# Kernel optimization log

Measured on AMD Instinct MI355X. Metric: run time of the kernel, lower is better.

Reference implementation:

```python
import jax, jax.numpy as jnp
import numpy as np
from math import sqrt

B, LT, LM = 4, 512, 1024
HID, NH, HD = 512, 8, 64          # self-attn: hidden, n_head, head_size
NHP, KS = 16, 64                  # cross-attn: 2*max_charge*n_head_per_mass, key_size
FF = 4 * HID
ALPHA = 2.0
EPS = 1e-5


def apply_rope(x, dis):
    # dis: same trailing dim as x; chunk into (sin, cos) halves
    s, c = jnp.split(dis, 2, axis=-1)
    x0, x1 = x[..., 0::2], x[..., 1::2]
    return jnp.concatenate([x0 * c - x1 * s, x1 * c + x0 * s], axis=-1)


def layer_norm(x, g, b):
    mu = jnp.mean(x, axis=-1, keepdims=True)
    var = jnp.mean(jnp.square(x - mu), axis=-1, keepdims=True)
    return (x - mu) * jax.lax.rsqrt(var + EPS) * g + b


def deep_norm(x, postx, g, b):
    # dropout is identity in eval mode
    return layer_norm(x * ALPHA + postx, g, b)


def attn_block(x_q, x_kv, dis_q, dis_k, wq, bq, wk, bk, wv, bv, wo, bo, mask, n_head, head_size):
    bsz = x_q.shape[0]
    q = (x_q @ wq.T + bq).reshape(bsz, -1, n_head, head_size)
    k = (x_kv @ wk.T + bk).reshape(bsz, -1, n_head, head_size)
    v = (x_kv @ wv.T + bv).reshape(bsz, -1, n_head, head_size)
    q = apply_rope(q, dis_q)
    k = apply_rope(k, dis_k)
    attn = jnp.einsum('bnhd,bmhd->bhnm', q, k) / sqrt(head_size)  # [B,H,Lq,Lk]
    attn = jnp.where(mask, attn, -jnp.inf)
    attn = jax.nn.softmax(attn, axis=-1)
    out = jnp.einsum('bhnm,bmhd->bnhd', attn, v).reshape(bsz, -1, n_head * head_size)
    return out @ wo.T + bo


def setup_inputs() -> dict:
    key = jax.random.key(0)
    ks = jax.random.split(key, 32)
    rn = lambda i, shape, s=1.0: jax.random.normal(ks[i], shape, jnp.float32) * s
    inp = {}
    inp['tgt'] = rn(0, (B, LT, HID))
    inp['mem'] = rn(1, (B, LM, HID))
    inp['glycan_mass'] = rn(2, (B, LT, NH, HD))
    inp['glycan_query_mass'] = rn(3, (B, LT, NH, HD))
    inp['glycan_crossattn_mass'] = rn(4, (B, LT, NHP, KS))
    inp['node_mass_emb'] = rn(5, (B, LM, NHP, KS))
    inp['node_mass'] = rn(6, (B, LM))
    causal = jnp.tril(jnp.ones((LT, LT), bool))
    inp['tgt_mask'] = jnp.broadcast_to(causal[None, None], (B, 1, LT, LT))
    inp['rel_mask'] = jnp.ones((B, 1, LT, LM), bool)
    inp['layer'] = 0
    inp['A'] = rn(7, (1,))
    w = 0.03  # param init scale
    # self-attn params
    inp['wq1'] = rn(8, (HID, HID), w);  inp['bq1'] = jnp.zeros((HID,))
    inp['wk1'] = rn(9, (HID, HID), w);  inp['bk1'] = jnp.zeros((HID,))
    inp['wv1'] = rn(10, (HID, HID), w); inp['bv1'] = jnp.zeros((HID,))
    inp['wo1'] = rn(11, (HID, HID), w); inp['bo1'] = jnp.zeros((HID,))
    inp['ln1_g'] = jnp.ones((HID,));    inp['ln1_b'] = jnp.zeros((HID,))
    # cross-attn params (projection dim NHP*KS = 1024)
    P = NHP * KS
    inp['wq2'] = rn(12, (P, HID), w);   inp['bq2'] = jnp.zeros((P,))
    inp['wk2'] = rn(13, (P, HID), w);   inp['bk2'] = jnp.zeros((P,))
    inp['wv2'] = rn(14, (P, HID), w);   inp['bv2'] = jnp.zeros((P,))
    inp['wo2'] = rn(15, (HID, P), w);   inp['bo2'] = jnp.zeros((HID,))
    inp['ln2_g'] = jnp.ones((HID,));    inp['ln2_b'] = jnp.zeros((HID,))
    # FFN params (no bias) + DeepNorm LN
    inp['w_ff1'] = rn(16, (FF, HID), w)
    inp['w_ff2'] = rn(17, (HID, FF), w)
    inp['ln3_g'] = jnp.ones((HID,));    inp['ln3_b'] = jnp.zeros((HID,))
    return inp


def reference(tgt, mem, glycan_mass, glycan_query_mass, glycan_crossattn_mass,
              node_mass_emb, node_mass, tgt_mask, rel_mask, layer, A,
              wq1, bq1, wk1, bk1, wv1, bv1, wo1, bo1, ln1_g, ln1_b,
              wq2, bq2, wk2, bk2, wv2, bv2, wo2, bo2, ln2_g, ln2_b,
              w_ff1, w_ff2, ln3_g, ln3_b):
    # masked self-attention with mass RoPE + DeepNorm
    postx = attn_block(tgt, tgt, glycan_query_mass, glycan_mass,
                       wq1, bq1, wk1, bk1, wv1, bv1, wo1, bo1,
                       tgt_mask, NH, HD)
    tgt = deep_norm(tgt, postx, ln1_g, ln1_b)
    # cross-attention with mass RoPE + DeepNorm (node_mass, layer, A unused in math)
    postx = attn_block(tgt, mem, glycan_crossattn_mass, node_mass_emb,
                       wq2, bq2, wk2, bk2, wv2, bv2, wo2, bo2,
                       rel_mask, NHP, KS)
    tgt = deep_norm(tgt, postx, ln2_g, ln2_b)
    # FFN + DeepNorm
    postx = jax.nn.relu(tgt @ w_ff1.T) @ w_ff2.T
    tgt = deep_norm(tgt, postx, ln3_g, ln3_b)
    return (tgt, A)
```

## Files before the change

kernel.cpp:

```cpp
#include <hip/hip_runtime.h>
#include <hip/hip_bf16.h>
#include <math.h>

#define EPS 1e-5f

typedef __attribute__((ext_vector_type(8))) __bf16 bf16x8;
typedef __attribute__((ext_vector_type(4))) float f32x4;

struct CvtJobs {
    const float* src[12];
    __bf16* dst[12];
    int off[13];
};

__global__ __launch_bounds__(256) void cvt_k(CvtJobs J, int total) {
    int g = blockIdx.x * 256 + threadIdx.x;
    if (g >= total) return;
    int j = 0;
    #pragma unroll
    for (int t = 0; t < 11; ++t) j += (g >= J.off[t + 1]) ? 1 : 0;
    int lg = g - J.off[j];
    const float* s = J.src[j] + (size_t)lg * 8;
    float4 a = *(const float4*)s;
    float4 b = *(const float4*)(s + 4);
    bf16x8 o;
    o[0] = (__bf16)a.x; o[1] = (__bf16)a.y; o[2] = (__bf16)a.z; o[3] = (__bf16)a.w;
    o[4] = (__bf16)b.x; o[5] = (__bf16)b.y; o[6] = (__bf16)b.z; o[7] = (__bf16)b.w;
    *(bf16x8*)(J.dst[j] + (size_t)lg * 8) = o;
}

template<int BT, int KS, typename OutT, bool RELU, bool HAS_BIAS, bool ROPE>
__global__ __launch_bounds__(256) void gemm_bf16_k(const __bf16* __restrict__ A,
                                                   const __bf16* __restrict__ W,
                                                   const float* __restrict__ b0,
                                                   const float* __restrict__ b1,
                                                   const float* __restrict__ b2,
                                                   int bshift,
                                                   const float* __restrict__ disK,
                                                   int ropeLo, int ropeHi, int dstride,
                                                   OutT* __restrict__ C,
                                                   int M, int N, int K) {
    constexpr int NI = BT / 32;
    __shared__ __bf16 As[BT * 64];
    __shared__ __bf16 Ws[BT * 64];

    const int tid  = threadIdx.x;
    const int wave = tid >> 6;
    const int lane = tid & 63;
    const int frow = lane & 15;
    const int fgrp = lane >> 4;

    const int nb  = gridDim.x * gridDim.y;
    const int bid = blockIdx.y * gridDim.x + blockIdx.x;
    const int v   = (bid & 7) * (nb >> 3) + (bid >> 3);
    const int bx  = (v % gridDim.x) * BT;
    const int by  = (v / gridDim.x) * BT;

    const int Kc = K / KS;
    const int kbeg = blockIdx.z * Kc;
    OutT* Cz = C + (size_t)blockIdx.z * M * N;

    const int wr = (wave >> 1) * (BT / 2);
    const int wc = (wave & 1) * (BT / 2);
    const int ldr = lane >> 3;
    const int ldc = (lane & 7) * 8;

    f32x4 acc[NI][NI] = {};

    for (int k0 = kbeg; k0 < kbeg + Kc; k0 += 64) {
        #pragma unroll
        for (int it = 0; it < NI; ++it) {
            int chunk = it * 4 + wave;
            int r = chunk * 8 + ldr;
            const __bf16* ga = A + (size_t)(by + r) * K + k0 + ldc;
            const __bf16* gw = W + (size_t)(bx + r) * K + k0 + ldc;
            __builtin_amdgcn_global_load_lds(
                (const __attribute__((address_space(1))) unsigned int*)ga,
                (__attribute__((address_space(3))) unsigned int*)(As + chunk * 512),
                16, 0, 0);
            __builtin_amdgcn_global_load_lds(
                (const __attribute__((address_space(1))) unsigned int*)gw,
                (__attribute__((address_space(3))) unsigned int*)(Ws + chunk * 512),
                16, 0, 0);
        }
        __syncthreads();

        #pragma unroll
        for (int kk = 0; kk < 2; ++kk) {
            bf16x8 af[NI], wf[NI];
            #pragma unroll
            for (int i = 0; i < NI; ++i)
                af[i] = *(const bf16x8*)&As[(wr + i * 16 + frow) * 64 + kk * 32 + fgrp * 8];
            #pragma unroll
            for (int j = 0; j < NI; ++j)
                wf[j] = *(const bf16x8*)&Ws[(wc + j * 16 + frow) * 64 + kk * 32 + fgrp * 8];
            #pragma unroll
            for (int i = 0; i < NI; ++i)
                #pragma unroll
                for (int j = 0; j < NI; ++j)
                    acc[i][j] = __builtin_amdgcn_mfma_f32_16x16x32_bf16(af[i], wf[j], acc[i][j], 0, 0, 0);
        }
        __syncthreads();
    }

    #pragma unroll
    for (int i = 0; i < NI; ++i) {
        #pragma unroll
        for (int jj = 0; jj < 4; ++jj) {
            int row = by + wr + i * 16 + fgrp * 4 + jj;
            #pragma unroll
            for (int j = 0; j < NI; ++j) {
                int col = bx + wc + j * 16 + frow;
                float val = acc[i][j][jj];
                if (HAS_BIAS) {
                    int sel = col >> bshift;
                    const float* bp = sel == 0 ? b0 : (sel == 1 ? b1 : b2);
                    val += bp[col & (int)((1u << bshift) - 1)];
                }
                if (RELU) val = fmaxf(val, 0.0f);
                if (ROPE && col >= ropeLo && col < ropeHi) {
                    int hcol = col & 63;
                    int p = hcol >> 1;
                    int hbase = col - hcol;
                    const float* dr = disK + (size_t)row * dstride + (hbase - ropeLo);
                    float sv = dr[p], cv = dr[32 + p];
                    float pv = __shfl_xor(val, 1);
                    val = ((col & 1) == 0) ? (val * cv - pv * sv)
                                           : (val * cv + pv * sv);
                }
                Cz[(size_t)row * N + col] = (OutT)val;
            }
        }
    }
}

template<int KS>
__global__ __launch_bounds__(256) void gemm_wo_k(const __bf16* __restrict__ Opart,
                                                 const float* __restrict__ lsums,
                                                 int prows, int H,
                                                 const __bf16* __restrict__ W,
                                                 float* __restrict__ C,
                                                 int M, int N, int K) {
    __shared__ __bf16 As[64 * 64];
    __shared__ __bf16 Ws[64 * 64];

    const int tid  = threadIdx.x;
    const int wave = tid >> 6;
    const int lane = tid & 63;
    const int frow = lane & 15;
    const int fgrp = lane >> 4;

    const int nb  = gridDim.x * gridDim.y;
    const int bid = blockIdx.y * gridDim.x + blockIdx.x;
    const int v   = (bid & 7) * (nb >> 3) + (bid >> 3);
    const int bx  = (v % gridDim.x) * 64;
    const int by  = (v / gridDim.x) * 64;

    const int Kc = K / KS;
    const int kbeg = blockIdx.z * Kc;
    float* Cz = C + (size_t)blockIdx.z * M * N;

    const int wr = (wave >> 1) * 32;
    const int wc = (wave & 1) * 32;
    const int ldr = lane >> 3;
    const int ldc = (lane & 7) * 8;

    f32x4 acc[2][2] = {};

    for (int k0 = kbeg; k0 < kbeg + Kc; k0 += 64) {
        const int h = k0 >> 6;
        #pragma unroll
        for (int it = 0; it < 2; ++it) {
            int chunk = it * 4 + wave;
            int r = chunk * 8 + ldr;
            size_t rid = (size_t)(by + r) * H + h;
            bf16x8 o0 = *(const bf16x8*)&Opart[rid * 64 + ldc];
            bf16x8 o1 = *(const bf16x8*)&Opart[((size_t)prows + rid) * 64 + ldc];
            float li = 1.0f / (lsums[rid] + lsums[prows + rid]);
            bf16x8 m;
            #pragma unroll
            for (int u = 0; u < 8; ++u)
                m[u] = (__bf16)(((float)o0[u] + (float)o1[u]) * li);
            *(bf16x8*)&As[chunk * 512 + lane * 8] = m;
            const __bf16* gw = W + (size_t)(bx + r) * K + k0 + ldc;
            __builtin_amdgcn_global_load_lds(
                (const __attribute__((address_space(1))) unsigned int*)gw,
                (__attribute__((address_space(3))) unsigned int*)(Ws + chunk * 512),
                16, 0, 0);
        }
        __syncthreads();

        #pragma unroll
        for (int kk = 0; kk < 2; ++kk) {
            bf16x8 af[2], wf[2];
            #pragma unroll
            for (int i = 0; i < 2; ++i)
                af[i] = *(const bf16x8*)&As[(wr + i * 16 + frow) * 64 + kk * 32 + fgrp * 8];
            #pragma unroll
            for (int j = 0; j < 2; ++j)
                wf[j] = *(const bf16x8*)&Ws[(wc + j * 16 + frow) * 64 + kk * 32 + fgrp * 8];
            #pragma unroll
            for (int i = 0; i < 2; ++i)
                #pragma unroll
                for (int j = 0; j < 2; ++j)
                    acc[i][j] = __builtin_amdgcn_mfma_f32_16x16x32_bf16(af[i], wf[j], acc[i][j], 0, 0, 0);
        }
        __syncthreads();
    }

    #pragma unroll
    for (int i = 0; i < 2; ++i)
        #pragma unroll
        for (int jj = 0; jj < 4; ++jj) {
            int row = by + wr + i * 16 + fgrp * 4 + jj;
            #pragma unroll
            for (int j = 0; j < 2; ++j) {
                int col = bx + wc + j * 16 + frow;
                Cz[(size_t)row * N + col] = acc[i][j][jj];
            }
        }
}

template<bool CAUSAL, int NSPLIT>
__global__ __launch_bounds__(256) void attn_bf16_k(const __bf16* __restrict__ Q,
                                                   const __bf16* __restrict__ K,
                                                   const __bf16* __restrict__ V,
                                                   const float* __restrict__ disQ,
                                                   __bf16* __restrict__ Opart,
                                                   float* __restrict__ lsums,
                                                   int H, int LQ, int LM,
                                                   int qstride, int kvstride,
                                                   int prows) {
    __shared__ __bf16 Ks[64 * 72];
    __shared__ __bf16 Vt[64 * 72];
    __shared__ __bf16 Ps[4 * 16 * 72];

    const int nqt = LQ >> 6;
    const int nb  = gridDim.x;
    const int bid = blockIdx.x;
    const int v   = (bid & 7) * (nb >> 3) + (bid >> 3);
    int t = v;
    const int qt = t % nqt; t /= nqt;
    const int chunk = t % NSPLIT; t /= NSPLIT;
    const int h = t % H;
    const int b = t / H;
    const int q0 = qt * 64;

    const int tid  = threadIdx.x;
    const int wave = tid >> 6;
    const int lane = tid & 63;
    const int frow = lane & 15;
    const int fgrp = lane >> 4;

    const int qrow = q0 + wave * 16 + frow;
    bf16x8 qf0, qf1;
    {
        const __bf16* qp = Q + ((size_t)b * LQ + qrow) * qstride + h * 64 + fgrp * 8;
        bf16x8 xa = *(const bf16x8*)qp;
        bf16x8 xb = *(const bf16x8*)(qp + 32);
        const float* dq = disQ + (((size_t)b * LQ + qrow) * H + h) * 64;
        #pragma unroll
        for (int u = 0; u < 4; ++u) {
            float sv = dq[fgrp * 4 + u], cv = dq[32 + fgrp * 4 + u];
            float x0 = (float)xa[2 * u], x1 = (float)xa[2 * u + 1];
            qf0[2 * u]     = (__bf16)(x0 * cv - x1 * sv);
            qf0[2 * u + 1] = (__bf16)(x1 * cv + x0 * sv);
            sv = dq[16 + fgrp * 4 + u]; cv = dq[48 + fgrp * 4 + u];
            x0 = (float)xb[2 * u]; x1 = (float)xb[2 * u + 1];
            qf1[2 * u]     = (__bf16)(x0 * cv - x1 * sv);
            qf1[2 * u + 1] = (__bf16)(x1 * cv + x0 * sv);
        }
    }

    f32x4 oacc[4] = {};
    float lsum[4] = {};

    const int kbAll = CAUSAL ? (qt + 1) : (LM >> 6);
    const int kcnt  = (LM >> 6) / NSPLIT;
    const int kb0   = chunk * kcnt;
    const int kb1   = min(kbAll, kb0 + kcnt);

    const int r   = tid >> 2;
    const int c0q = tid & 3;
    const int kphys = (r & 7) + 8 * ((r >> 3) ^ (2 * c0q));

    for (int kb = kb0; kb < kb1; ++kb) {
        const int m0 = kb * 64;
        {
            const __bf16* kp = K + ((size_t)b * LM + m0 + r) * kvstride + h * 64 + c0q * 16;
            *(bf16x8*)&Ks[r * 72 + c0q * 16]     = *(const bf16x8*)kp;
            *(bf16x8*)&Ks[r * 72 + c0q * 16 + 8] = *(const bf16x8*)(kp + 8);
        }
        {
            const __bf16* vp = V + ((size_t)b * LM + m0 + r) * kvstride + h * 64 + c0q * 16;
            bf16x8 va = *(const bf16x8*)vp;
            bf16x8 vb = *(const bf16x8*)(vp + 8);
            #pragma unroll
            for (int j = 0; j < 8; ++j) {
                Vt[(c0q * 16 + j) * 72 + kphys]     = va[j];
                Vt[(c0q * 16 + 8 + j) * 72 + kphys] = vb[j];
            }
        }
        __syncthreads();

        f32x4 s[4];
        #pragma unroll
        for (int n = 0; n < 4; ++n) {
            bf16x8 kf0 = *(const bf16x8*)&Ks[(n * 16 + frow) * 72 + fgrp * 8];
            bf16x8 kf1 = *(const bf16x8*)&Ks[(n * 16 + frow) * 72 + 32 + fgrp * 8];
            f32x4 tt = {0.f, 0.f, 0.f, 0.f};
            tt = __builtin_amdgcn_mfma_f32_16x16x32_bf16(qf0, kf0, tt, 0, 0, 0);
            tt = __builtin_amdgcn_mfma_f32_16x16x32_bf16(qf1, kf1, tt, 0, 0, 0);
            s[n] = tt;
        }

        #pragma unroll
        for (int n = 0; n < 4; ++n)
            #pragma unroll
            for (int jj = 0; jj < 4; ++jj) {
                bool valid = (!CAUSAL) ||
                    ((m0 + n * 16 + frow) <= (q0 + wave * 16 + fgrp * 4 + jj));
                s[n][jj] = valid ? __expf(s[n][jj] * 0.125f - 8.0f) : 0.0f;
            }

        #pragma unroll
        for (int jj = 0; jj < 4; ++jj) {
            float rs = (s[0][jj] + s[1][jj]) + (s[2][jj] + s[3][jj]);
            #pragma unroll
            for (int msk = 8; msk >= 1; msk >>= 1) rs += __shfl_xor(rs, msk);
            lsum[jj] += rs;
        }

        #pragma unroll
        for (int n = 0; n < 4; ++n)
            #pragma unroll
            for (int jj = 0; jj < 4; ++jj) {
                int q = fgrp * 4 + jj;
                int kidx = (frow & 7) + 8 * (((2 * n) + (frow >> 3)) ^ (2 * ((q >> 3) & 1)));
                Ps[wave * 1152 + q * 72 + kidx] = (__bf16)s[n][jj];
            }

        #pragma unroll
        for (int c = 0; c < 2; ++c) {
            int pblk = (c * 4 + fgrp) ^ (2 * ((frow >> 3) & 1));
            bf16x8 pf = *(const bf16x8*)&Ps[wave * 1152 + frow * 72 + 8 * pblk];
            #pragma unroll
            for (int n = 0; n < 4; ++n) {
                int vblk = (c * 4 + fgrp) ^ (2 * n);
                bf16x8 vf = *(const bf16x8*)&Vt[(n * 16 + frow) * 72 + 8 * vblk];
                oacc[n] = __builtin_amdgcn_mfma_f32_16x16x32_bf16(pf, vf, oacc[n], 0, 0, 0);
            }
        }
        __syncthreads();
    }

    #pragma unroll
    for (int jj = 0; jj < 4; ++jj) {
        int q = q0 + wave * 16 + fgrp * 4 + jj;
        size_t ridx = (size_t)chunk * prows + ((size_t)b * LQ + q) * H + h;
        if (frow == 0) lsums[ridx] = lsum[jj];
        #pragma unroll
        for (int n = 0; n < 4; ++n)
            Opart[ridx * 64 + n * 16 + frow] = (__bf16)oacc[n][jj];
    }
}

template<int NP, bool HASB, bool WRITE_BF>
__global__ __launch_bounds__(256) void deepnorm_k(const float* __restrict__ x,
                                                  const float* __restrict__ p0,
                                                  const float* __restrict__ p1,
                                                  const float* __restrict__ p2,
                                                  const float* __restrict__ p3,
                                                  const float* __restrict__ bias,
                                                  const float* __restrict__ g,
                                                  const float* __restrict__ b,
                                                  float* __restrict__ out,
                                                  __bf16* __restrict__ out_bf,
                                                  const float* __restrict__ Ain,
                                                  float* __restrict__ Aout) {
    int row = blockIdx.x;
    int tid = threadIdx.x;
    if (Aout && row == 0 && tid == 0) Aout[0] = Ain[0];
    size_t i0 = (size_t)row * 512 + tid, i1 = i0 + 256;
    float a0 = p0[i0], a1 = p0[i1];
    if (NP > 1) { a0 += p1[i0]; a1 += p1[i1]; }
    if (NP > 2) { a0 += p2[i0]; a1 += p2[i1]; }
    if (NP > 3) { a0 += p3[i0]; a1 += p3[i1]; }
    if (HASB)   { a0 += bias[tid]; a1 += bias[tid + 256]; }
    float v0 = x[i0] * 2.0f + a0;
    float v1 = x[i1] * 2.0f + a1;

    __shared__ float red[4];
    int wave = tid >> 6, lane = tid & 63;

    float s = v0 + v1;
    #pragma unroll
    for (int o = 32; o >= 1; o >>= 1) s += __shfl_xor(s, o);
    if (lane == 0) red[wave] = s;
    __syncthreads();
    float mean = (red[0] + red[1] + red[2] + red[3]) * (1.0f / 512.0f);

    float d0 = v0 - mean, d1 = v1 - mean;
    float vs = d0 * d0 + d1 * d1;
    #pragma unroll
    for (int o = 32; o >= 1; o >>= 1) vs += __shfl_xor(vs, o);
    __syncthreads();
    if (lane == 0) red[wave] = vs;
    __syncthreads();
    float var = (red[0] + red[1] + red[2] + red[3]) * (1.0f / 512.0f);
    float inv = rsqrtf(var + EPS);

    float o0 = d0 * inv * g[tid] + b[tid];
    float o1 = d1 * inv * g[tid + 256] + b[tid + 256];
    out[i0] = o0;
    out[i1] = o1;
    if (WRITE_BF) {
        out_bf[i0] = (__bf16)o0;
        out_bf[i1] = (__bf16)o1;
    }
}

extern "C" void kernel_launch(void* const* d_in, const int* in_sizes, int n_in,
                              void* d_out, int out_size, void* d_ws, size_t ws_size,
                              hipStream_t stream) {
    const float* tgt  = (const float*)d_in[0];
    const float* mem  = (const float*)d_in[1];
    const float* dis_k1 = (const float*)d_in[2];
    const float* dis_q1 = (const float*)d_in[3];
    const float* dis_q2 = (const float*)d_in[4];
    const float* dis_k2 = (const float*)d_in[5];
    const float* A_in   = (const float*)d_in[10];
    const float* wq1 = (const float*)d_in[11]; const float* bq1 = (const float*)d_in[12];
    const float* wk1 = (const float*)d_in[13]; const float* bk1 = (const float*)d_in[14];
    const float* wv1 = (const float*)d_in[15]; const float* bv1 = (const float*)d_in[16];
    const float* wo1 = (const float*)d_in[17]; const float* bo1 = (const float*)d_in[18];
    const float* ln1g = (const float*)d_in[19]; const float* ln1b = (const float*)d_in[20];
    const float* wq2 = (const float*)d_in[21]; const float* bq2 = (const float*)d_in[22];
    const float* wk2 = (const float*)d_in[23]; const float* bk2 = (const float*)d_in[24];
    const float* wv2 = (const float*)d_in[25]; const float* bv2 = (const float*)d_in[26];
    const float* wo2 = (const float*)d_in[27]; const float* bo2 = (const float*)d_in[28];
    const float* ln2g = (const float*)d_in[29]; const float* ln2b = (const float*)d_in[30];
    const float* wff1 = (const float*)d_in[31]; const float* wff2 = (const float*)d_in[32];
    const float* ln3g = (const float*)d_in[33]; const float* ln3b = (const float*)d_in[34];

    char* ws = (char*)d_ws;
    auto MB = [&](size_t mb) { return ws + mb * 1024 * 1024; };

    __bf16* wqkv1_bf = (__bf16*)MB(0);
    __bf16* wo1_bf   = (__bf16*)MB(2);
    __bf16* wq2_bf   = (__bf16*)MB(3);
    __bf16* wkv2_bf  = (__bf16*)MB(4);
    __bf16* wo2_bf   = (__bf16*)MB(6);
    __bf16* wff1_bf  = (__bf16*)MB(7);
    __bf16* wff2_bf  = (__bf16*)MB(9);
    __bf16* tgt_bf   = (__bf16*)MB(11);
    __bf16* mem_bf   = (__bf16*)MB(13);
    __bf16* qkv1_bf  = (__bf16*)MB(17);
    __bf16* Opart    = (__bf16*)MB(25);
    float*  x1       = (float*)MB(41);
    float*  post0    = (float*)MB(45);
    float*  post1    = (float*)MB(49);
    float*  post2    = (float*)MB(53);
    float*  post3    = (float*)MB(57);
    __bf16* kv2_bf   = (__bf16*)MB(45);
    float*  x2       = (float*)MB(61);
    __bf16* x2_bf    = (__bf16*)MB(65);
    float*  lsums    = (float*)MB(67);
    __bf16* x1_bf    = tgt_bf;
    __bf16* q2_bf    = qkv1_bf;
    __bf16* ffh_bf   = Opart;

    float* out = (float*)d_out;

    CvtJobs J;
    const float* srcs[12] = {tgt, mem, wq1, wk1, wv1, wo1, wq2, wk2, wv2, wo2, wff1, wff2};
    __bf16* dsts[12] = {tgt_bf, mem_bf, wqkv1_bf, wqkv1_bf + 262144, wqkv1_bf + 524288,
                        wo1_bf, wq2_bf, wkv2_bf, wkv2_bf + 524288, wo2_bf, wff1_bf, wff2_bf};
    int sizes[12] = {2048 * 512, 4096 * 512, 512 * 512, 512 * 512, 512 * 512, 512 * 512,
                     1024 * 512, 1024 * 512, 1024 * 512, 1024 * 512, 2048 * 512, 512 * 2048};
    int acc = 0;
    for (int i = 0; i < 12; ++i) { J.src[i] = srcs[i]; J.dst[i] = dsts[i]; J.off[i] = acc; acc += sizes[i] / 8; }
    J.off[12] = acc;
    cvt_k<<<(acc + 255) / 256, 256, 0, stream>>>(J, acc);

    gemm_bf16_k<64, 1, __bf16, false, true, true><<<dim3(24, 32), 256, 0, stream>>>(
        tgt_bf, wqkv1_bf, bq1, bk1, bv1, 9, dis_k1, 512, 1024, 512,
        qkv1_bf, 2048, 1536, 512);
    attn_bf16_k<true, 2><<<512, 256, 0, stream>>>(qkv1_bf, qkv1_bf + 512, qkv1_bf + 1024,
                                                  dis_q1, Opart, lsums,
                                                  8, 512, 512, 1536, 1536, 16384);
    gemm_wo_k<2><<<dim3(8, 32, 2), 256, 0, stream>>>(Opart, lsums, 16384, 8,
                                                     wo1_bf, post0, 2048, 512, 512);
    deepnorm_k<2, true, true><<<2048, 256, 0, stream>>>(tgt, post0, post1, nullptr, nullptr,
                                                        bo1, ln1g, ln1b, x1, x1_bf,
                                                        nullptr, nullptr);

    gemm_bf16_k<64, 1, __bf16, false, true, false><<<dim3(16, 32), 256, 0, stream>>>(
        x1_bf, wq2_bf, bq2, bq2, bq2, 31, nullptr, 0, 0, 0,
        q2_bf, 2048, 1024, 512);
    gemm_bf16_k<64, 1, __bf16, false, true, true><<<dim3(32, 64), 256, 0, stream>>>(
        mem_bf, wkv2_bf, bk2, bv2, bv2, 10, dis_k2, 0, 1024, 1024,
        kv2_bf, 4096, 2048, 512);
    attn_bf16_k<false, 2><<<1024, 256, 0, stream>>>(q2_bf, kv2_bf, kv2_bf + 1024,
                                                    dis_q2, Opart, lsums,
                                                    16, 512, 1024, 1024, 2048, 32768);
    gemm_wo_k<2><<<dim3(8, 32, 2), 256, 0, stream>>>(Opart, lsums, 32768, 16,
                                                     wo2_bf, post0, 2048, 512, 1024);
    deepnorm_k<2, true, true><<<2048, 256, 0, stream>>>(x1, post0, post1, nullptr, nullptr,
                                                        bo2, ln2g, ln2b, x2, x2_bf,
                                                        nullptr, nullptr);

    gemm_bf16_k<64, 1, __bf16, true, false, false><<<dim3(32, 32), 256, 0, stream>>>(
        x2_bf, wff1_bf, nullptr, nullptr, nullptr, 31, nullptr, 0, 0, 0,
        ffh_bf, 2048, 2048, 512);
    gemm_bf16_k<64, 4, float, false, false, false><<<dim3(8, 32, 4), 256, 0, stream>>>(
        ffh_bf, wff2_bf, nullptr, nullptr, nullptr, 31, nullptr, 0, 0, 0,
        post0, 2048, 512, 2048);
    deepnorm_k<4, false, false><<<2048, 256, 0, stream>>>(x2, post0, post1, post2, post3,
                                                          nullptr, ln3g, ln3b, out, nullptr,
                                                          A_in, out + 2048 * 512);
}
```

Baseline: 176.3 us.

## Merge self-attn QKV and cross-attn KV projections into one dual-GEMM launch

Pulls the GEMM body out into a device function and adds a dual kernel that runs the self-attention QKV projection and the memory KV projection in one grid, choosing the problem by block index. The cross-attention KV projection now runs before self-attention, which saves a launch and fills the GPU with more blocks at once. The FF2 split-K factor also drops from 4 to 2 so the final deepnorm reduces fewer partials, and workspace buffers are moved so kv2 no longer overlaps post0/post1. The trade-off is a larger combined grid, and FF2 now has less parallelism from split-K.

```diff
diff --git a/kernel.cpp b/kernel.cpp
--- a/kernel.cpp
+++ b/kernel.cpp
@@ -29,17 +29,17 @@
     *(bf16x8*)(J.dst[j] + (size_t)lg * 8) = o;
 }
 
-template<int BT, int KS, typename OutT, bool RELU, bool HAS_BIAS, bool ROPE>
-__global__ __launch_bounds__(256) void gemm_bf16_k(const __bf16* __restrict__ A,
-                                                   const __bf16* __restrict__ W,
-                                                   const float* __restrict__ b0,
-                                                   const float* __restrict__ b1,
-                                                   const float* __restrict__ b2,
-                                                   int bshift,
-                                                   const float* __restrict__ disK,
-                                                   int ropeLo, int ropeHi, int dstride,
-                                                   OutT* __restrict__ C,
-                                                   int M, int N, int K) {
+template<int BT, typename OutT, bool RELU, bool HAS_BIAS, bool ROPE>
+__device__ __forceinline__ void gemm_body(const __bf16* __restrict__ A,
+                                          const __bf16* __restrict__ W,
+                                          const float* b0, const float* b1, const float* b2,
+                                          int bshift,
+                                          const float* disK,
+                                          int ropeLo, int ropeHi, int dstride,
+                                          OutT* __restrict__ C,
+                                          int M, int N, int K,
+                                          int bid, int nb, int gx,
+                                          int kbeg, int kend) {
     constexpr int NI = BT / 32;
     __shared__ __bf16 As[BT * 64];
     __shared__ __bf16 Ws[BT * 64];
@@ -50,15 +50,9 @@
     const int frow = lane & 15;
     const int fgrp = lane >> 4;
 
-    const int nb  = gridDim.x * gridDim.y;
-    const int bid = blockIdx.y * gridDim.x + blockIdx.x;
     const int v   = (bid & 7) * (nb >> 3) + (bid >> 3);
-    const int bx  = (v % gridDim.x) * BT;
-    const int by  = (v / gridDim.x) * BT;
-
-    const int Kc = K / KS;
-    const int kbeg = blockIdx.z * Kc;
-    OutT* Cz = C + (size_t)blockIdx.z * M * N;
+    const int bx  = (v % gx) * BT;
+    const int by  = (v / gx) * BT;
 
     const int wr = (wave >> 1) * (BT / 2);
     const int wc = (wave & 1) * (BT / 2);
@@ -67,7 +61,7 @@
 
     f32x4 acc[NI][NI] = {};
 
-    for (int k0 = kbeg; k0 < kbeg + Kc; k0 += 64) {
+    for (int k0 = kbeg; k0 < kend; k0 += 64) {
         #pragma unroll
         for (int it = 0; it < NI; ++it) {
             int chunk = it * 4 + wave;
@@ -128,10 +122,50 @@
                     val = ((col & 1) == 0) ? (val * cv - pv * sv)
                                            : (val * cv + pv * sv);
                 }
-                Cz[(size_t)row * N + col] = (OutT)val;
+                C[(size_t)row * N + col] = (OutT)val;
             }
         }
     }
+}
+
+template<int BT, int KS, typename OutT, bool RELU, bool HAS_BIAS, bool ROPE>
+__global__ __launch_bounds__(256) void gemm_bf16_k(const __bf16* __restrict__ A,
+                                                   const __bf16* __restrict__ W,
+                                                   const float* b0, const float* b1,
+                                                   const float* b2, int bshift,
+                                                   const float* disK,
+                                                   int ropeLo, int ropeHi, int dstride,
+                                                   OutT* __restrict__ C,
+                                                   int M, int N, int K) {
+    const int nb  = gridDim.x * gridDim.y;
+    const int bid = blockIdx.y * gridDim.x + blockIdx.x;
+    const int Kc  = K / KS;
+    const int kbeg = blockIdx.z * Kc;
+    OutT* Cz = C + (size_t)blockIdx.z * M * N;
+    gemm_body<BT, OutT, RELU, HAS_BIAS, ROPE>(A, W, b0, b1, b2, bshift,
+                                              disK, ropeLo, ropeHi, dstride,
+                                              Cz, M, N, K, bid, nb, gridDim.x,
+                                              kbeg, kbeg + Kc);
+}
+
+struct GemmP {
+    const __bf16* A;
+    const __bf16* W;
+    const float *b0, *b1, *b2;
+    const float* disK;
+    __bf16* C;
+    int bshift, ropeLo, ropeHi, dstride;
+    int M, N, K, gx, nb;
+};
+
+__global__ __launch_bounds__(256) void gemm_dual_k(GemmP p0, GemmP p1, int nb0) {
+    int bid = blockIdx.x;
+    const GemmP& p = (bid < nb0) ? p0 : p1;
+    int lb = (bid < nb0) ? bid : bid - nb0;
+    gemm_body<64, __bf16, false, true, true>(p.A, p.W, p.b0, p.b1, p.b2, p.bshift,
+                                             p.disK, p.ropeLo, p.ropeHi, p.dstride,
+                                             p.C, p.M, p.N, p.K, lb, p.nb, p.gx,
+                                             0, p.K);
 }
 
 template<int KS>
@@ -456,16 +490,14 @@
     __bf16* tgt_bf   = (__bf16*)MB(11);
     __bf16* mem_bf   = (__bf16*)MB(13);
     __bf16* qkv1_bf  = (__bf16*)MB(17);
-    __bf16* Opart    = (__bf16*)MB(25);
-    float*  x1       = (float*)MB(41);
-    float*  post0    = (float*)MB(45);
-    float*  post1    = (float*)MB(49);
-    float*  post2    = (float*)MB(53);
-    float*  post3    = (float*)MB(57);
-    __bf16* kv2_bf   = (__bf16*)MB(45);
-    float*  x2       = (float*)MB(61);
-    __bf16* x2_bf    = (__bf16*)MB(65);
-    float*  lsums    = (float*)MB(67);
+    __bf16* Opart    = (__bf16*)MB(23);
+    float*  x1       = (float*)MB(31);
+    float*  post0    = (float*)MB(35);
+    float*  post1    = (float*)MB(39);
+    __bf16* kv2_bf   = (__bf16*)MB(43);
+    float*  x2       = (float*)MB(59);
+    __bf16* x2_bf    = (__bf16*)MB(63);
+    float*  lsums    = (float*)MB(65);
     __bf16* x1_bf    = tgt_bf;
     __bf16* q2_bf    = qkv1_bf;
     __bf16* ffh_bf   = Opart;
@@ -483,9 +515,17 @@
     J.off[12] = acc;
     cvt_k<<<(acc + 255) / 256, 256, 0, stream>>>(J, acc);
 
-    gemm_bf16_k<64, 1, __bf16, false, true, true><<<dim3(24, 32), 256, 0, stream>>>(
-        tgt_bf, wqkv1_bf, bq1, bk1, bv1, 9, dis_k1, 512, 1024, 512,
-        qkv1_bf, 2048, 1536, 512);
+    GemmP p0, p1;
+    p0.A = tgt_bf;  p0.W = wqkv1_bf; p0.b0 = bq1; p0.b1 = bk1; p0.b2 = bv1;
+    p0.disK = dis_k1; p0.C = qkv1_bf;
+    p0.bshift = 9; p0.ropeLo = 512; p0.ropeHi = 1024; p0.dstride = 512;
+    p0.M = 2048; p0.N = 1536; p0.K = 512; p0.gx = 24; p0.nb = 768;
+    p1.A = mem_bf;  p1.W = wkv2_bf;  p1.b0 = bk2; p1.b1 = bv2; p1.b2 = bv2;
+    p1.disK = dis_k2; p1.C = kv2_bf;
+    p1.bshift = 10; p1.ropeLo = 0; p1.ropeHi = 1024; p1.dstride = 1024;
+    p1.M = 4096; p1.N = 2048; p1.K = 512; p1.gx = 32; p1.nb = 2048;
+    gemm_dual_k<<<768 + 2048, 256, 0, stream>>>(p0, p1, 768);
+
     attn_bf16_k<true, 2><<<512, 256, 0, stream>>>(qkv1_bf, qkv1_bf + 512, qkv1_bf + 1024,
                                                   dis_q1, Opart, lsums,
                                                   8, 512, 512, 1536, 1536, 16384);
@@ -498,9 +538,6 @@
     gemm_bf16_k<64, 1, __bf16, false, true, false><<<dim3(16, 32), 256, 0, stream>>>(
         x1_bf, wq2_bf, bq2, bq2, bq2, 31, nullptr, 0, 0, 0,
         q2_bf, 2048, 1024, 512);
-    gemm_bf16_k<64, 1, __bf16, false, true, true><<<dim3(32, 64), 256, 0, stream>>>(
-        mem_bf, wkv2_bf, bk2, bv2, bv2, 10, dis_k2, 0, 1024, 1024,
-        kv2_bf, 4096, 2048, 512);
     attn_bf16_k<false, 2><<<1024, 256, 0, stream>>>(q2_bf, kv2_bf, kv2_bf + 1024,
                                                     dis_q2, Opart, lsums,
                                                     16, 512, 1024, 1024, 2048, 32768);
@@ -513,10 +550,10 @@
     gemm_bf16_k<64, 1, __bf16, true, false, false><<<dim3(32, 32), 256, 0, stream>>>(
         x2_bf, wff1_bf, nullptr, nullptr, nullptr, 31, nullptr, 0, 0, 0,
         ffh_bf, 2048, 2048, 512);
-    gemm_bf16_k<64, 4, float, false, false, false><<<dim3(8, 32, 4), 256, 0, stream>>>(
+    gemm_bf16_k<64, 2, float, false, false, false><<<dim3(8, 32, 2), 256, 0, stream>>>(
         ffh_bf, wff2_bf, nullptr, nullptr, nullptr, 31, nullptr, 0, 0, 0,
         post0, 2048, 512, 2048);
-    deepnorm_k<4, false, false><<<2048, 256, 0, stream>>>(x2, post0, post1, post2, post3,
+    deepnorm_k<2, false, false><<<2048, 256, 0, stream>>>(x2, post0, post1, nullptr, nullptr,
                                                           nullptr, ln3g, ln3b, out, nullptr,
                                                           A_in, out + 2048 * 512);
 }
```

Result: faster. 166.3 us (-5.6%).
